# Optimization experiments

Measured on AMD Instinct MI355X. Metric: run time of the kernel, lower is better.

## Reference

```python
import jax, jax.numpy as jnp
import numpy as np

N_NODES = 100000
N_EDGES = 3200000
N_IN = 5
N_OUT = 16


def setup_inputs() -> dict:
    key = jax.random.key(0)
    k1, k2, k3, k4 = jax.random.split(key, 4)
    atom = jax.random.normal(k1, (N_NODES, N_IN), dtype=jnp.float32)
    edge_index = jax.random.randint(k2, (2, N_EDGES), 0, N_NODES, dtype=jnp.int64)
    # Linear(n_input=5, n_neural=16) parameters
    W = jax.random.normal(k3, (N_OUT, N_IN), dtype=jnp.float32) / np.sqrt(N_IN)
    b = jax.random.normal(k4, (N_OUT,), dtype=jnp.float32) * 0.01
    return {"atom": atom, "edge_index": edge_index, "W": W, "b": b}


def reference(atom, edge_index, W, b):
    n = atom.shape[0]
    # add_self_loops
    loops = jnp.arange(n, dtype=edge_index.dtype)
    row = jnp.concatenate([edge_index[0], loops])  # source nodes [E+N]
    col = jnp.concatenate([edge_index[1], loops])  # target nodes [E+N]
    # x = Linear(atom)
    x = atom @ W.T + b  # [N, n_out]
    # degree over target index (includes self loops -> deg >= 1)
    deg = jax.ops.segment_sum(jnp.ones_like(col, dtype=x.dtype), col, num_segments=n)
    dis = deg ** -0.5  # deg_inv_sqrt, finite since deg >= 1
    norm = dis[row] * dis[col]  # [E+N]
    # gather-scale-scatter: message = norm * x_j, aggr='add' at col
    msgs = norm[:, None] * x[row]  # [E+N, n_out]
    out = jax.ops.segment_sum(msgs, col, num_segments=n)  # [N, n_out]
    return jax.nn.relu(out)
```

## Files before the change

kernel.cpp:

```cpp
#include <hip/hip_runtime.h>

#define N_IN 5
#define N_OUT 16
#define NB 256
#define BN 400
#define CAP 14336
#define QSCALE 1024.0f
#define QBIAS 8192
#define BIN_MAGIC 10737419ull

__device__ __forceinline__ int bin_of(int c) {
    return (int)(((unsigned long long)(unsigned)c * BIN_MAGIC) >> 32);
}

__global__ __launch_bounds__(1024) void partition_kernel(
        const int* __restrict__ row, const int* __restrict__ col,
        int e, int* __restrict__ eb, int* __restrict__ cursor) {
    __shared__ int hist[NB];
    __shared__ int base[NB];
    const int tid = threadIdx.x;
    const int e4 = e >> 2;
    const int nper = (e4 + (int)gridDim.x - 1) / (int)gridDim.x;
    const int b0 = (int)blockIdx.x * nper;
    int lim = e4 - b0; if (lim > nper) lim = nper; if (lim < 0) lim = 0;
    const int4* rowv = (const int4*)row;
    const int4* colv = (const int4*)col;

    if (tid < NB) hist[tid] = 0;
    __syncthreads();

    int pay[4][4];
    int met[4][4];
    bool val[4];
#pragma unroll
    for (int k = 0; k < 4; ++k) {
        val[k] = (tid + k * 1024) < lim;
        if (val[k]) {
            const int idx = b0 + tid + k * 1024;
            int4 r4 = rowv[idx];
            int4 c4 = colv[idx];
            int cc[4] = {c4.x, c4.y, c4.z, c4.w};
            int rr[4] = {r4.x, r4.y, r4.z, r4.w};
#pragma unroll
            for (int j = 0; j < 4; ++j) {
                int b = bin_of(cc[j]);
                int pr = atomicAdd(&hist[b], 1);
                pay[k][j] = ((cc[j] - b * BN) << 17) | rr[j];
                met[k][j] = (b << 14) | pr;
            }
        }
    }
    __syncthreads();
    if (tid < NB) {
        int h = hist[tid];
        base[tid] = h ? atomicAdd(&cursor[tid], h) : 0;
    }
    __syncthreads();
#pragma unroll
    for (int k = 0; k < 4; ++k) {
        if (val[k]) {
#pragma unroll
            for (int j = 0; j < 4; ++j) {
                int b = met[k][j] >> 14;
                int p = base[b] + (met[k][j] & 16383);
                if (p < CAP)
                    eb[b * CAP + p] = pay[k][j];
            }
        }
    }
    if (blockIdx.x == 0) {
        for (int k = (e4 << 2) + tid; k < e; k += 1024) {
            int c = col[k];
            int b = bin_of(c);
            int o = atomicAdd(&cursor[b], 1);
            if (o < CAP) eb[b * CAP + o] = ((c - b * BN) << 17) | row[k];
        }
    }
}

__global__ __launch_bounds__(1024) void deg_quant_kernel(
        const int* __restrict__ eb, const int* __restrict__ cursor,
        const float* __restrict__ atom,
        ulonglong2* __restrict__ qdatom, unsigned short* __restrict__ deg16,
        int n) {
    __shared__ int hist[BN];
    int bin = blockIdx.x;
    if (threadIdx.x < BN) hist[threadIdx.x] = 0;
    __syncthreads();
    int s0 = bin * CAP;
    int cnt = min(max(cursor[bin], 0), CAP);
    const int4* ebv = (const int4*)(eb + s0);
    int cnt4 = cnt >> 2;
    for (int i = threadIdx.x; i < cnt4; i += 1024) {
        int4 v = ebv[i];
        atomicAdd(&hist[v.x >> 17], 1);
        atomicAdd(&hist[v.y >> 17], 1);
        atomicAdd(&hist[v.z >> 17], 1);
        atomicAdd(&hist[v.w >> 17], 1);
    }
    for (int i = (cnt4 << 2) + (int)threadIdx.x; i < cnt; i += 1024)
        atomicAdd(&hist[eb[s0 + i] >> 17], 1);
    __syncthreads();
    int l = threadIdx.x;
    if (l >= BN) return;
    int node = bin * BN + l;
    if (node >= n) return;
    int deg = hist[l];
    deg16[node] = (unsigned short)deg;
    float d = rsqrtf((float)(deg + 1));
    const float* ap = atom + (size_t)node * N_IN;
    unsigned long long f[6];
#pragma unroll
    for (int k = 0; k < 5; ++k) {
        int q = __float2int_rn(d * ap[k] * QSCALE);
        q = min(max(q, -8191), 8191);
        f[k] = (unsigned long long)(q + QBIAS);
    }
    f[5] = (unsigned long long)(__float2int_rn(d * QSCALE) + QBIAS);
    ulonglong2 v;
    v.x = f[0] | (f[1] << 21) | (f[2] << 42);
    v.y = f[3] | (f[4] << 21) | (f[5] << 42);
    qdatom[node] = v;
}

__global__ __launch_bounds__(1024) void accum_final(
        const int* __restrict__ eb, const int* __restrict__ cursor,
        const ulonglong2* __restrict__ qdatom,
        const unsigned short* __restrict__ deg16,
        const float* __restrict__ atom,
        const float* __restrict__ W, const float* __restrict__ bias,
        float* __restrict__ out, int n) {
    __shared__ unsigned long long accA[BN];
    __shared__ unsigned long long accB[BN];
    int bin = blockIdx.x;
    if (threadIdx.x < BN) { accA[threadIdx.x] = 0ull; accB[threadIdx.x] = 0ull; }
    __syncthreads();
    int s0 = bin * CAP;
    int cnt = min(max(cursor[bin], 0), CAP);
    const int4* ebv = (const int4*)(eb + s0);
    int cnt4 = cnt >> 2;
    for (int i = threadIdx.x; i < cnt4; i += 1024) {
        int4 v = ebv[i];
        ulonglong2 q0 = qdatom[v.x & 0x1FFFF];
        ulonglong2 q1 = qdatom[v.y & 0x1FFFF];
        ulonglong2 q2 = qdatom[v.z & 0x1FFFF];
        ulonglong2 q3 = qdatom[v.w & 0x1FFFF];
        atomicAdd(&accA[v.x >> 17], q0.x);
        atomicAdd(&accB[v.x >> 17], q0.y);
        atomicAdd(&accA[v.y >> 17], q1.x);
        atomicAdd(&accB[v.y >> 17], q1.y);
        atomicAdd(&accA[v.z >> 17], q2.x);
        atomicAdd(&accB[v.z >> 17], q2.y);
        atomicAdd(&accA[v.w >> 17], q3.x);
        atomicAdd(&accB[v.w >> 17], q3.y);
    }
    for (int i = (cnt4 << 2) + (int)threadIdx.x; i < cnt; i += 1024) {
        int v = eb[s0 + i];
        ulonglong2 q = qdatom[v & 0x1FFFF];
        atomicAdd(&accA[v >> 17], q.x);
        atomicAdd(&accB[v >> 17], q.y);
    }
    __syncthreads();
    int l = threadIdx.x;
    if (l >= BN) return;
    int node = bin * BN + l;
    if (node >= n) return;
    unsigned long long SA = accA[l], SB = accB[l];
    int deg = deg16[node];
    int db = deg * QBIAS;
    const float inv = 1.0f / QSCALE;
    float s[6];
    s[0] = (float)((int)((SA      ) & 0x1FFFFF) - db) * inv;
    s[1] = (float)((int)((SA >> 21) & 0x1FFFFF) - db) * inv;
    s[2] = (float)((int)((SA >> 42) & 0x1FFFFF) - db) * inv;
    s[3] = (float)((int)((SB      ) & 0x1FFFFF) - db) * inv;
    s[4] = (float)((int)((SB >> 21) & 0x1FFFFF) - db) * inv;
    s[5] = (float)((int)((SB >> 42) & 0x1FFFFF) - db) * inv;
    float d = rsqrtf((float)(deg + 1));
    const float* ap = atom + (size_t)node * N_IN;
    float t5[5];
#pragma unroll
    for (int k = 0; k < 5; ++k) t5[k] = d * (s[k] + d * ap[k]);
    float t1 = d * (s[5] + d);
    float ov[N_OUT];
#pragma unroll
    for (int o = 0; o < N_OUT; ++o) {
        float a = bias[o] * t1;
#pragma unroll
        for (int k = 0; k < 5; ++k) a = fmaf(W[o * N_IN + k], t5[k], a);
        ov[o] = fmaxf(a, 0.0f);
    }
    float4* op = (float4*)(out + (size_t)node * N_OUT);
#pragma unroll
    for (int q = 0; q < 4; ++q)
        op[q] = make_float4(ov[4 * q], ov[4 * q + 1], ov[4 * q + 2], ov[4 * q + 3]);
}

extern "C" void kernel_launch(void* const* d_in, const int* in_sizes, int n_in,
                              void* d_out, int out_size, void* d_ws, size_t ws_size,
                              hipStream_t stream) {
    const float* atom = (const float*)d_in[0];
    const int*   eidx = (const int*)d_in[1];
    const float* W    = (const float*)d_in[2];
    const float* b    = (const float*)d_in[3];
    float* out = (float*)d_out;

    int n = in_sizes[0] / N_IN;
    int e = in_sizes[1] / 2;
    const int* row = eidx;
    const int* col = eidx + e;

    auto align256 = [](size_t v) { return (v + 255) & ~(size_t)255; };
    char* w = (char*)d_ws;
    int*            cursor = (int*)w;            w += align256(NB * 4);
    int*            eb     = (int*)w;            w += align256((size_t)NB * CAP * 4);
    ulonglong2*     qdatom = (ulonglong2*)w;     w += align256((size_t)NB * BN * 16);
    unsigned short* deg16  = (unsigned short*)w;

    hipMemsetAsync(cursor, 0, NB * sizeof(int), stream);
    partition_kernel<<<256, 1024, 0, stream>>>(row, col, e, eb, cursor);
    deg_quant_kernel<<<NB, 1024, 0, stream>>>(eb, cursor, atom, qdatom, deg16, n);
    accum_final<<<NB, 1024, 0, stream>>>(eb, cursor, qdatom, deg16, atom, W, b, out, n);
}
```

Baseline: 119.9 us.

## Replace global-cursor bin partition with per-chunk fixed-size cells

Each partition block now writes its edges straight into a private 128-slot cell per bin, indexed by the shared-memory histogram position. This removes the global cursor atomics, the second sync/scatter pass and the memset. Consumer kernels read 256 cells per bin, four threads per cell, and mask the tail of each quad. The cost is a larger scratch buffer, less contiguous reads, and silent edge dropping if any chunk-bin cell overflows 128 entries (mean is about 49).

```diff
diff --git a/kernel.cpp b/kernel.cpp
--- a/kernel.cpp
+++ b/kernel.cpp
@@ -4,7 +4,8 @@
 #define N_OUT 16
 #define NB 256
 #define BN 400
-#define CAP 14336
+#define NCH 256
+#define CELL 128
 #define QSCALE 1024.0f
 #define QBIAS 8192
 #define BIN_MAGIC 10737419ull
@@ -15,28 +16,25 @@
 
 __global__ __launch_bounds__(1024) void partition_kernel(
         const int* __restrict__ row, const int* __restrict__ col,
-        int e, int* __restrict__ eb, int* __restrict__ cursor) {
+        int e, int* __restrict__ eb, int* __restrict__ cnts) {
     __shared__ int hist[NB];
-    __shared__ int base[NB];
     const int tid = threadIdx.x;
     const int e4 = e >> 2;
-    const int nper = (e4 + (int)gridDim.x - 1) / (int)gridDim.x;
+    const int nper = (e4 + NCH - 1) / NCH;
     const int b0 = (int)blockIdx.x * nper;
     int lim = e4 - b0; if (lim > nper) lim = nper; if (lim < 0) lim = 0;
+    const int cbase = (int)blockIdx.x * NB;
     const int4* rowv = (const int4*)row;
     const int4* colv = (const int4*)col;
 
     if (tid < NB) hist[tid] = 0;
     __syncthreads();
 
-    int pay[4][4];
-    int met[4][4];
-    bool val[4];
 #pragma unroll
     for (int k = 0; k < 4; ++k) {
-        val[k] = (tid + k * 1024) < lim;
-        if (val[k]) {
-            const int idx = b0 + tid + k * 1024;
+        const int t = tid + k * 1024;
+        if (t < lim) {
+            const int idx = b0 + t;
             int4 r4 = rowv[idx];
             int4 c4 = colv[idx];
             int cc[4] = {c4.x, c4.y, c4.z, c4.w};
@@ -45,26 +43,8 @@
             for (int j = 0; j < 4; ++j) {
                 int b = bin_of(cc[j]);
                 int pr = atomicAdd(&hist[b], 1);
-                pay[k][j] = ((cc[j] - b * BN) << 17) | rr[j];
-                met[k][j] = (b << 14) | pr;
-            }
-        }
-    }
-    __syncthreads();
-    if (tid < NB) {
-        int h = hist[tid];
-        base[tid] = h ? atomicAdd(&cursor[tid], h) : 0;
-    }
-    __syncthreads();
-#pragma unroll
-    for (int k = 0; k < 4; ++k) {
-        if (val[k]) {
-#pragma unroll
-            for (int j = 0; j < 4; ++j) {
-                int b = met[k][j] >> 14;
-                int p = base[b] + (met[k][j] & 16383);
-                if (p < CAP)
-                    eb[b * CAP + p] = pay[k][j];
+                if (pr < CELL)
+                    eb[((cbase + b) << 7) + pr] = ((cc[j] - b * BN) << 17) | rr[j];
             }
         }
     }
@@ -72,38 +52,41 @@
         for (int k = (e4 << 2) + tid; k < e; k += 1024) {
             int c = col[k];
             int b = bin_of(c);
-            int o = atomicAdd(&cursor[b], 1);
-            if (o < CAP) eb[b * CAP + o] = ((c - b * BN) << 17) | row[k];
-        }
-    }
+            int pr = atomicAdd(&hist[b], 1);
+            if (pr < CELL)
+                eb[((cbase + b) << 7) + pr] = ((c - b * BN) << 17) | row[k];
+        }
+    }
+    __syncthreads();
+    if (tid < NB) cnts[cbase + tid] = min(hist[tid], CELL);
 }
 
 __global__ __launch_bounds__(1024) void deg_quant_kernel(
-        const int* __restrict__ eb, const int* __restrict__ cursor,
+        const int* __restrict__ eb, const int* __restrict__ cnts,
         const float* __restrict__ atom,
         ulonglong2* __restrict__ qdatom, unsigned short* __restrict__ deg16,
         int n) {
     __shared__ int hist[BN];
-    int bin = blockIdx.x;
-    if (threadIdx.x < BN) hist[threadIdx.x] = 0;
-    __syncthreads();
-    int s0 = bin * CAP;
-    int cnt = min(max(cursor[bin], 0), CAP);
-    const int4* ebv = (const int4*)(eb + s0);
-    int cnt4 = cnt >> 2;
-    for (int i = threadIdx.x; i < cnt4; i += 1024) {
-        int4 v = ebv[i];
-        atomicAdd(&hist[v.x >> 17], 1);
-        atomicAdd(&hist[v.y >> 17], 1);
-        atomicAdd(&hist[v.z >> 17], 1);
-        atomicAdd(&hist[v.w >> 17], 1);
-    }
-    for (int i = (cnt4 << 2) + (int)threadIdx.x; i < cnt; i += 1024)
-        atomicAdd(&hist[eb[s0 + i] >> 17], 1);
-    __syncthreads();
-    int l = threadIdx.x;
+    const int bin = blockIdx.x;
+    const int tid = threadIdx.x;
+    if (tid < BN) hist[tid] = 0;
+    __syncthreads();
+    const int c = tid >> 2, sub = tid & 3;
+    const int cnt = cnts[c * NB + bin];
+    const int4* cell = (const int4*)(eb + (((size_t)c * NB + bin) << 7));
+    const int quads = (cnt + 3) >> 2;
+    for (int q = sub; q < quads; q += 4) {
+        int4 v = cell[q];
+        int base = q << 2;
+        if (base + 0 < cnt) atomicAdd(&hist[v.x >> 17], 1);
+        if (base + 1 < cnt) atomicAdd(&hist[v.y >> 17], 1);
+        if (base + 2 < cnt) atomicAdd(&hist[v.z >> 17], 1);
+        if (base + 3 < cnt) atomicAdd(&hist[v.w >> 17], 1);
+    }
+    __syncthreads();
+    const int l = tid;
     if (l >= BN) return;
-    int node = bin * BN + l;
+    const int node = bin * BN + l;
     if (node >= n) return;
     int deg = hist[l];
     deg16[node] = (unsigned short)deg;
@@ -124,7 +107,7 @@
 }
 
 __global__ __launch_bounds__(1024) void accum_final(
-        const int* __restrict__ eb, const int* __restrict__ cursor,
+        const int* __restrict__ eb, const int* __restrict__ cnts,
         const ulonglong2* __restrict__ qdatom,
         const unsigned short* __restrict__ deg16,
         const float* __restrict__ atom,
@@ -132,38 +115,42 @@
         float* __restrict__ out, int n) {
     __shared__ unsigned long long accA[BN];
     __shared__ unsigned long long accB[BN];
-    int bin = blockIdx.x;
-    if (threadIdx.x < BN) { accA[threadIdx.x] = 0ull; accB[threadIdx.x] = 0ull; }
-    __syncthreads();
-    int s0 = bin * CAP;
-    int cnt = min(max(cursor[bin], 0), CAP);
-    const int4* ebv = (const int4*)(eb + s0);
-    int cnt4 = cnt >> 2;
-    for (int i = threadIdx.x; i < cnt4; i += 1024) {
-        int4 v = ebv[i];
-        ulonglong2 q0 = qdatom[v.x & 0x1FFFF];
-        ulonglong2 q1 = qdatom[v.y & 0x1FFFF];
-        ulonglong2 q2 = qdatom[v.z & 0x1FFFF];
-        ulonglong2 q3 = qdatom[v.w & 0x1FFFF];
-        atomicAdd(&accA[v.x >> 17], q0.x);
-        atomicAdd(&accB[v.x >> 17], q0.y);
-        atomicAdd(&accA[v.y >> 17], q1.x);
-        atomicAdd(&accB[v.y >> 17], q1.y);
-        atomicAdd(&accA[v.z >> 17], q2.x);
-        atomicAdd(&accB[v.z >> 17], q2.y);
-        atomicAdd(&accA[v.w >> 17], q3.x);
-        atomicAdd(&accB[v.w >> 17], q3.y);
-    }
-    for (int i = (cnt4 << 2) + (int)threadIdx.x; i < cnt; i += 1024) {
-        int v = eb[s0 + i];
-        ulonglong2 q = qdatom[v & 0x1FFFF];
-        atomicAdd(&accA[v >> 17], q.x);
-        atomicAdd(&accB[v >> 17], q.y);
-    }
-    __syncthreads();
-    int l = threadIdx.x;
+    const int bin = blockIdx.x;
+    const int tid = threadIdx.x;
+    if (tid < BN) { accA[tid] = 0ull; accB[tid] = 0ull; }
+    __syncthreads();
+    const int c = tid >> 2, sub = tid & 3;
+    const int cnt = cnts[c * NB + bin];
+    const int4* cell = (const int4*)(eb + (((size_t)c * NB + bin) << 7));
+    const int quads = (cnt + 3) >> 2;
+    for (int q = sub; q < quads; q += 4) {
+        int4 v = cell[q];
+        int base = q << 2;
+        if (base + 0 < cnt) {
+            ulonglong2 q0 = qdatom[v.x & 0x1FFFF];
+            atomicAdd(&accA[v.x >> 17], q0.x);
+            atomicAdd(&accB[v.x >> 17], q0.y);
+        }
+        if (base + 1 < cnt) {
+            ulonglong2 q1 = qdatom[v.y & 0x1FFFF];
+            atomicAdd(&accA[v.y >> 17], q1.x);
+            atomicAdd(&accB[v.y >> 17], q1.y);
+        }
+        if (base + 2 < cnt) {
+            ulonglong2 q2 = qdatom[v.z & 0x1FFFF];
+            atomicAdd(&accA[v.z >> 17], q2.x);
+            atomicAdd(&accB[v.z >> 17], q2.y);
+        }
+        if (base + 3 < cnt) {
+            ulonglong2 q3 = qdatom[v.w & 0x1FFFF];
+            atomicAdd(&accA[v.w >> 17], q3.x);
+            atomicAdd(&accB[v.w >> 17], q3.y);
+        }
+    }
+    __syncthreads();
+    const int l = tid;
     if (l >= BN) return;
-    int node = bin * BN + l;
+    const int node = bin * BN + l;
     if (node >= n) return;
     unsigned long long SA = accA[l], SB = accB[l];
     int deg = deg16[node];
@@ -212,13 +199,12 @@
 
     auto align256 = [](size_t v) { return (v + 255) & ~(size_t)255; };
     char* w = (char*)d_ws;
-    int*            cursor = (int*)w;            w += align256(NB * 4);
-    int*            eb     = (int*)w;            w += align256((size_t)NB * CAP * 4);
-    ulonglong2*     qdatom = (ulonglong2*)w;     w += align256((size_t)NB * BN * 16);
+    int*            eb     = (int*)w;         w += align256((size_t)NCH * NB * CELL * 4);
+    int*            cnts   = (int*)w;         w += align256((size_t)NCH * NB * 4);
+    ulonglong2*     qdatom = (ulonglong2*)w;  w += align256((size_t)NB * BN * 16);
     unsigned short* deg16  = (unsigned short*)w;
 
-    hipMemsetAsync(cursor, 0, NB * sizeof(int), stream);
-    partition_kernel<<<256, 1024, 0, stream>>>(row, col, e, eb, cursor);
-    deg_quant_kernel<<<NB, 1024, 0, stream>>>(eb, cursor, atom, qdatom, deg16, n);
-    accum_final<<<NB, 1024, 0, stream>>>(eb, cursor, qdatom, deg16, atom, W, b, out, n);
-}
+    partition_kernel<<<NCH, 1024, 0, stream>>>(row, col, e, eb, cnts);
+    deg_quant_kernel<<<NB, 1024, 0, stream>>>(eb, cnts, atom, qdatom, deg16, n);
+    accum_final<<<NB, 1024, 0, stream>>>(eb, cnts, qdatom, deg16, atom, W, b, out, n);
+}
```

After: 115.9 us (median of 2 runs). 3.4% less time.
